# Optimization experiments

Hardware: AMD Instinct MI355X
Metric: run time of the kernel (lower is better)

Reference implementation:

```python
import jax, jax.numpy as jnp
import numpy as np

N_NODES = 10000
LN_EPS = 1e-5


def _gcn(x, W, b, src, dst):
    # GraphConvolution: linear transform then sum-aggregate messages over edges.
    sup = x @ W                               # [B, N, H]
    msg = sup[:, src, :]                      # [B, E, H] gather from source nodes
    agg = jax.vmap(lambda m: jax.ops.segment_sum(m, dst, num_segments=N_NODES))(msg)
    return agg + b


def _layernorm(x, g, b):
    mu = jnp.mean(x, axis=-1, keepdims=True)
    var = jnp.var(x, axis=-1, keepdims=True)
    return (x - mu) * jax.lax.rsqrt(var + LN_EPS) * g + b


def _attention_pool(x, W, u, num_iterations=3):
    # x: [B, N, d] -> r: [B, 1, d]
    a = jnp.tanh(x @ W) @ u                   # [B, N]
    alpha = jax.nn.softmax(a, axis=1)
    r = jnp.einsum('bn,bnd->bd', alpha, x)
    for _ in range(num_iterations):
        beta = jax.nn.softmax(jnp.einsum('bnd,bd->bn', x, r), axis=1)
        r = jnp.einsum('bn,bnd->bd', beta, x)
    return r[:, None, :]


def _forward(x, src, dst, W_conv0, b_conv0, W_convs, b_convs,
             mW1, mb1, mW2, mb2, mW3, mb3,
             ln1_g, ln1_b, ln2_g, ln2_b, attnW, attnu, fW1, fb1, fW2, fb2,
             fcW, fcb):
    gelu = lambda t: jax.nn.gelu(t, approximate=False)
    # stacked GCN layers (first layer distinct input dim)
    x = gelu(_gcn(x, W_conv0, b_conv0, src, dst))
    for i in range(W_convs.shape[0]):
        x = gelu(_gcn(x, W_convs[i], b_convs[i], src, dst))
    # dropout is identity in eval mode
    # MLP head
    x = jax.nn.relu(x @ mW1 + mb1)
    x = jax.nn.relu(x @ mW2 + mb2)
    x = x @ mW3 + mb3
    # Encoder: 2 layers of (attention-pool residual + LN + FFN residual + LN)
    for i in range(2):
        x = x + _attention_pool(x, attnW[i], attnu[i])   # broadcast [B,1,d]
        x = _layernorm(x, ln1_g[i], ln1_b[i])
        h = jax.nn.relu(x @ fW1[i] + fb1[i]) @ fW2[i] + fb2[i]
        x = _layernorm(x + h, ln2_g[i], ln2_b[i])
    x = x @ fcW + fcb                          # [B, N, out]
    return x.mean(axis=1)                      # [B, out]


def setup_inputs() -> dict:
    key = jax.random.key(0)
    ks = jax.random.split(key, 32)
    B, N, E = 4, N_NODES, 160000
    F_in, H, D, A, OUT = 128, 256, 256, 8, 10
    s = lambda k, *shape: jax.random.normal(k, shape, jnp.float32) * 0.05
    return {
        'x': jax.random.normal(ks[0], (B, N, F_in), jnp.float32),
        'src': jax.random.randint(ks[1], (E,), 0, N, jnp.int32),
        'dst': jax.random.randint(ks[2], (E,), 0, N, jnp.int32),
        'W_conv0': s(ks[3], F_in, H), 'b_conv0': s(ks[4], H),
        'W_convs': s(ks[5], 3, H, H), 'b_convs': s(ks[6], 3, H),
        'mW1': s(ks[7], H, H // 2), 'mb1': s(ks[8], H // 2),
        'mW2': s(ks[9], H // 2, H // 4), 'mb2': s(ks[10], H // 4),
        'mW3': s(ks[11], H // 4, D), 'mb3': s(ks[12], D),
        'ln1_g': jnp.ones((2, D), jnp.float32), 'ln1_b': jnp.zeros((2, D), jnp.float32),
        'ln2_g': jnp.ones((2, D), jnp.float32), 'ln2_b': jnp.zeros((2, D), jnp.float32),
        'attnW': s(ks[13], 2, D, A), 'attnu': s(ks[14], 2, A),
        'fW1': s(ks[15], 2, D, H), 'fb1': s(ks[16], 2, H),
        'fW2': s(ks[17], 2, H, D), 'fb2': s(ks[18], 2, D),
        'fcW': s(ks[19], D, OUT), 'fcb': s(ks[20], OUT),
    }


def reference(x, src, dst, W_conv0, b_conv0, W_convs, b_convs,
              mW1, mb1, mW2, mb2, mW3, mb3,
              ln1_g, ln1_b, ln2_g, ln2_b, attnW, attnu, fW1, fb1, fW2, fb2,
              fcW, fcb):
    return _forward(x, src, dst, W_conv0, b_conv0, W_convs, b_convs,
                    mW1, mb1, mW2, mb2, mW3, mb3,
                    ln1_g, ln1_b, ln2_g, ln2_b, attnW, attnu, fW1, fb1, fW2, fb2,
                    fcW, fcb)
```

## Files before the change

kernel.cpp:

```cpp
#include <hip/hip_runtime.h>
#include <math.h>

#define NN 10000
#define NB 4
#define NE 160000
#define DM 256
#define MR (NB * NN)
#define LN_EPS 1e-5f
#define PCH 40
#define NCH (NN / PCH)
#define CCH 100

typedef __attribute__((ext_vector_type(8))) short short8;
typedef __attribute__((ext_vector_type(4))) float floatx4;
typedef __attribute__((ext_vector_type(2))) float f32x2;


__device__ inline float bf2f(unsigned short u) {
    unsigned int x = ((unsigned int)u) << 16;
    float f;
    __builtin_memcpy(&f, &x, 4);
    return f;
}

__device__ inline unsigned short f2bf(float f) {
    unsigned int x;
    __builtin_memcpy(&x, &f, 4);
    unsigned int r = x + 0x7FFFu + ((x >> 16) & 1u);
    return (unsigned short)(r >> 16);
}

__device__ inline float gelu_exact(float x) {
    return 0.5f * x * (1.0f + erff(x * 0.70710678118654752f));
}

__device__ inline float waveAllReduce(float v) {
#pragma unroll
    for (int off = 32; off > 0; off >>= 1) v += __shfl_xor(v, off, 64);
    return v;
}

__device__ inline float group16Reduce(float v) {
#pragma unroll
    for (int off = 8; off > 0; off >>= 1) v += __shfl_xor(v, off, 64);
    return v;
}

__device__ inline void gld16(const unsigned short* g, unsigned short* l) {
    __builtin_amdgcn_global_load_lds((const __attribute__((address_space(1))) void*)g,
                                     (__attribute__((address_space(3))) void*)l, 16, 0, 0);
}


__global__ void zero_i32_kernel(int* p, int n) {
    int i = blockIdx.x * 256 + threadIdx.x;
    if (i < n) p[i] = 0;
}

__global__ void cvt_bf16_kernel(const float* __restrict__ in, unsigned short* __restrict__ out, int n) {
    int i = blockIdx.x * 256 + threadIdx.x;
    if (i < n) out[i] = f2bf(in[i]);
}

struct TD { const float* src; unsigned short* dst; int K; int N; };
struct TDs { TD d[11]; };

__global__ void transpose_all_kernel(TDs tds) {
    TD t = tds.d[blockIdx.y];
    int idx = blockIdx.x * 256 + threadIdx.x;
    int total = t.K * t.N;
    if (idx < total) {
        int n = idx / t.K;
        int k = idx - n * t.K;
        t.dst[idx] = f2bf(t.src[(size_t)k * t.N + n]);
    }
}


__global__ void hist_kernel(const int* __restrict__ dst, int* __restrict__ counts, int e) {
    int i = blockIdx.x * 256 + threadIdx.x;
    if (i < e) atomicAdd(&counts[dst[i]], 1);
}

__global__ __launch_bounds__(256) void scan_kernel(const int* __restrict__ counts,
                                                   int* __restrict__ row_ptr,
                                                   int* __restrict__ fill_pos, int n) {
    __shared__ int sums[256];
    int tid = threadIdx.x;
    int chunk = (n + 255) / 256;
    int s0 = tid * chunk;
    int s1 = min(n, s0 + chunk);
    int local = 0;
    for (int i = s0; i < s1; i++) local += counts[i];
    sums[tid] = local;
    __syncthreads();
    for (int off = 1; off < 256; off <<= 1) {
        int v = (tid >= off) ? sums[tid - off] : 0;
        __syncthreads();
        sums[tid] += v;
        __syncthreads();
    }
    int base = (tid == 0) ? 0 : sums[tid - 1];
    for (int i = s0; i < s1; i++) {
        row_ptr[i] = base;
        fill_pos[i] = base;
        base += counts[i];
    }
    if (tid == 255) row_ptr[n] = sums[255];
}

__global__ void fill_kernel(const int* __restrict__ src, const int* __restrict__ dst,
                            int* __restrict__ fill_pos, int* __restrict__ csr_boff, int e) {
    int i = blockIdx.x * 256 + threadIdx.x;
    if (i < e) {
        int p = atomicAdd(&fill_pos[dst[i]], 1);
        csr_boff[p] = src[i] * (NB * DM * 2);
    }
}


template <int BN, int CM, int K>
__global__ __launch_bounds__(256) void mfma_gemm_kernel(
    const unsigned short* __restrict__ A, const unsigned short* __restrict__ Bt,
    const float* __restrict__ bias, void* __restrict__ Cp, int N, int act) {
    constexpr int NBF = BN / 32;
    constexpr int NI = K / 32;
    __shared__ unsigned short AsL[2][4 * 64 * 8];
    __shared__ unsigned short BsL[2][(BN / 16) * 64 * 8];

    const int tid = threadIdx.x;
    const int w = tid >> 6, l = tid & 63;
    const int wm = w >> 1, wn = w & 1;
    const int bm0 = blockIdx.y * 64;
    const int bn0 = blockIdx.x * BN;
    const int lm = l & 15, lq = l >> 4;

    floatx4 acc[2][NBF];
#pragma unroll
    for (int mi = 0; mi < 2; mi++)
#pragma unroll
        for (int ni = 0; ni < NBF; ni++) acc[mi][ni] = (floatx4){0.f, 0.f, 0.f, 0.f};

    const int a_row = bm0 + (tid >> 6) * 16 + (l & 15);
    const int s_kc = (l >> 4) * 8;
    int b_rown[BN / 64], b_kc[BN / 64];
#pragma unroll
    for (int cc = 0; cc < BN / 64; cc++) {
        int c = tid + cc * 256;
        b_rown[cc] = bn0 + (c >> 6) * 16 + (c & 15);
        b_kc[cc] = ((c & 63) >> 4) * 8;
    }

    gld16(&A[(size_t)a_row * K + s_kc], &AsL[0][tid * 8]);
#pragma unroll
    for (int cc = 0; cc < BN / 64; cc++) {
        int c = tid + cc * 256;
        gld16(&Bt[(size_t)b_rown[cc] * K + b_kc[cc]], &BsL[0][c * 8]);
    }

#pragma unroll
    for (int i = 0; i < NI; i++) {
        const int buf = i & 1;
        __syncthreads();
        if (i + 1 < NI) {
            int k0 = (i + 1) * 32;
            gld16(&A[(size_t)a_row * K + k0 + s_kc], &AsL[buf ^ 1][tid * 8]);
#pragma unroll
            for (int cc = 0; cc < BN / 64; cc++) {
                int c = tid + cc * 256;
                gld16(&Bt[(size_t)b_rown[cc] * K + k0 + b_kc[cc]], &BsL[buf ^ 1][c * 8]);
            }
        }
        short8 af[2], bfv[NBF];
#pragma unroll
        for (int mi = 0; mi < 2; mi++) af[mi] = *(short8*)&AsL[buf][((wm * 2 + mi) * 64 + l) * 8];
#pragma unroll
        for (int ni = 0; ni < NBF; ni++) bfv[ni] = *(short8*)&BsL[buf][((wn * NBF + ni) * 64 + l) * 8];
#pragma unroll
        for (int mi = 0; mi < 2; mi++)
#pragma unroll
            for (int ni = 0; ni < NBF; ni++)
                acc[mi][ni] = __builtin_amdgcn_mfma_f32_16x16x32_bf16(af[mi], bfv[ni], acc[mi][ni], 0, 0, 0);
    }

#pragma unroll
    for (int ni = 0; ni < NBF; ni++) {
        int col = bn0 + (wn * NBF + ni) * 16 + lm;
        float bv = bias ? bias[col] : 0.0f;
#pragma unroll
        for (int mi = 0; mi < 2; mi++) {
            int row0 = bm0 + (wm * 2 + mi) * 16 + lq * 4;
#pragma unroll
            for (int r = 0; r < 4; r++) {
                int row = row0 + r;
                float v = acc[mi][ni][r] + bv;
                if (act == 1) v = fmaxf(v, 0.0f);
                if (CM == 0) {
                    ((float*)Cp)[(size_t)row * N + col] = v;
                } else if (CM == 1) {
                    ((unsigned short*)Cp)[(size_t)row * N + col] = f2bf(v);
                } else {
                    int bb = row / NN;
                    int nn = row - bb * NN;
                    ((unsigned short*)Cp)[(size_t)nn * (NB * DM) + bb * DM + col] = f2bf(v);
                }
            }
        }
    }
}


__global__ __launch_bounds__(256) void gemm_ln_kernel(
    const unsigned short* __restrict__ A,
    const unsigned short* __restrict__ Bt,
    const float* __restrict__ bias,
    const unsigned short* __restrict__ x1,
    const float* __restrict__ g, const float* __restrict__ bt,
    unsigned short* __restrict__ out16) {
    constexpr int K = 256, NBF = 8, NI = K / 32;
    __shared__ unsigned short AsL[2][4 * 64 * 8];
    __shared__ unsigned short BsL[2][16 * 64 * 8];
    __shared__ float rs[2][64], rq[2][64];

    const int tid = threadIdx.x;
    const int w = tid >> 6, l = tid & 63;
    const int wm = w >> 1, wn = w & 1;
    const int bm0 = blockIdx.x * 64;
    const int lm = l & 15, lq = l >> 4;

    floatx4 acc[2][NBF];
#pragma unroll
    for (int mi = 0; mi < 2; mi++)
#pragma unroll
        for (int ni = 0; ni < NBF; ni++) acc[mi][ni] = (floatx4){0.f, 0.f, 0.f, 0.f};

    const int a_row = bm0 + (tid >> 6) * 16 + (l & 15);
    const int s_kc = (l >> 4) * 8;
    int b_rown[4], b_kc[4];
#pragma unroll
    for (int cc = 0; cc < 4; cc++) {
        int c = tid + cc * 256;
        b_rown[cc] = (c >> 6) * 16 + (c & 15);
        b_kc[cc] = ((c & 63) >> 4) * 8;
    }

    gld16(&A[(size_t)a_row * K + s_kc], &AsL[0][tid * 8]);
#pragma unroll
    for (int cc = 0; cc < 4; cc++) {
        int c = tid + cc * 256;
        gld16(&Bt[(size_t)b_rown[cc] * K + b_kc[cc]], &BsL[0][c * 8]);
    }

#pragma unroll
    for (int i = 0; i < NI; i++) {
        const int buf = i & 1;
        __syncthreads();
        if (i + 1 < NI) {
            int k0 = (i + 1) * 32;
            gld16(&A[(size_t)a_row * K + k0 + s_kc], &AsL[buf ^ 1][tid * 8]);
#pragma unroll
            for (int cc = 0; cc < 4; cc++) {
                int c = tid + cc * 256;
                gld16(&Bt[(size_t)b_rown[cc] * K + k0 + b_kc[cc]], &BsL[buf ^ 1][c * 8]);
            }
        }
        short8 af[2], bfv[NBF];
#pragma unroll
        for (int mi = 0; mi < 2; mi++) af[mi] = *(short8*)&AsL[buf][((wm * 2 + mi) * 64 + l) * 8];
#pragma unroll
        for (int ni = 0; ni < NBF; ni++) bfv[ni] = *(short8*)&BsL[buf][((wn * NBF + ni) * 64 + l) * 8];
#pragma unroll
        for (int mi = 0; mi < 2; mi++)
#pragma unroll
            for (int ni = 0; ni < NBF; ni++)
                acc[mi][ni] = __builtin_amdgcn_mfma_f32_16x16x32_bf16(af[mi], bfv[ni], acc[mi][ni], 0, 0, 0);
    }

    float fb[NBF], gv[NBF], bv[NBF];
#pragma unroll
    for (int ni = 0; ni < NBF; ni++) {
        int col = (wn * NBF + ni) * 16 + lm;
        fb[ni] = bias[col];
        gv[ni] = g[col];
        bv[ni] = bt[col];
    }
    float psum[2][4], psq[2][4];
#pragma unroll
    for (int mi = 0; mi < 2; mi++)
#pragma unroll
        for (int r = 0; r < 4; r++) { psum[mi][r] = 0.f; psq[mi][r] = 0.f; }

#pragma unroll
    for (int mi = 0; mi < 2; mi++) {
        int row0 = bm0 + (wm * 2 + mi) * 16 + lq * 4;
#pragma unroll
        for (int r = 0; r < 4; r++) {
#pragma unroll
            for (int ni = 0; ni < NBF; ni++) {
                int col = (wn * NBF + ni) * 16 + lm;
                float y = bf2f(x1[(size_t)(row0 + r) * DM + col]) + acc[mi][ni][r] + fb[ni];
                acc[mi][ni][r] = y;
                psum[mi][r] += y;
                psq[mi][r] += y * y;
            }
        }
    }
#pragma unroll
    for (int mi = 0; mi < 2; mi++)
#pragma unroll
        for (int r = 0; r < 4; r++) {
            float s = group16Reduce(psum[mi][r]);
            float q = group16Reduce(psq[mi][r]);
            if (lm == 0) {
                int rl = (wm * 2 + mi) * 16 + lq * 4 + r;
                rs[wn][rl] = s;
                rq[wn][rl] = q;
            }
        }
    __syncthreads();
#pragma unroll
    for (int mi = 0; mi < 2; mi++) {
        int row0 = bm0 + (wm * 2 + mi) * 16 + lq * 4;
#pragma unroll
        for (int r = 0; r < 4; r++) {
            int rl = (wm * 2 + mi) * 16 + lq * 4 + r;
            float s = rs[0][rl] + rs[1][rl];
            float q = rq[0][rl] + rq[1][rl];
            float mean = s * (1.0f / 256.0f);
            float var = q * (1.0f / 256.0f) - mean * mean;
            float rstd = rsqrtf(var + LN_EPS);
#pragma unroll
            for (int ni = 0; ni < NBF; ni++) {
                int col = (wn * NBF + ni) * 16 + lm;
                out16[(size_t)(row0 + r) * DM + col] =
                    f2bf((acc[mi][ni][r] - mean) * rstd * gv[ni] + bv[ni]);
            }
        }
    }
}


__global__ __launch_bounds__(256) void agg_kernel(const unsigned short* __restrict__ sup,
                                                  const int* __restrict__ row_ptr,
                                                  const int* __restrict__ csr_boff,
                                                  const float* __restrict__ bias,
                                                  unsigned short* __restrict__ out) {
    const char* supc = (const char*)sup;
    int slice = blockIdx.x & 7;
    int grp = blockIdx.x >> 3;
    int w = threadIdx.x >> 6, l = threadIdx.x & 63;
    int n = grp * 4 + w;
    int s = __builtin_amdgcn_readfirstlane(row_ptr[n]);
    int e = __builtin_amdgcn_readfirstlane(row_ptr[n + 1]);
    const int lane_off = slice * 256 + l * 4;
    f32x2 acc = {0.f, 0.f};
    int j = s;
    for (; j + 8 <= e; j += 8) {
        int off[8];
#pragma unroll
        for (int k = 0; k < 8; k++) off[k] = csr_boff[j + k];
        unsigned int v[8];
#pragma unroll
        for (int k = 0; k < 8; k++)
            v[k] = *(const unsigned int*)(supc + (unsigned)(off[k] + lane_off));
#pragma unroll
        for (int k = 0; k < 8; k++) {
            unsigned int lo = v[k] << 16;
            unsigned int hi = v[k] & 0xFFFF0000u;
            float fx, fy;
            __builtin_memcpy(&fx, &lo, 4);
            __builtin_memcpy(&fy, &hi, 4);
            f32x2 t = {fx, fy};
            acc += t;
        }
    }
    for (; j < e; j++) {
        unsigned int v = *(const unsigned int*)(supc + (unsigned)(csr_boff[j] + lane_off));
        unsigned int lo = v << 16;
        unsigned int hi = v & 0xFFFF0000u;
        float fx, fy;
        __builtin_memcpy(&fx, &lo, 4);
        __builtin_memcpy(&fy, &hi, 4);
        f32x2 t = {fx, fy};
        acc += t;
    }
    int gdim = slice * 128 + l * 2;
    int b = gdim >> 8;
    int d = gdim & 255;
    float2 bv = *(const float2*)&bias[d];
    ushort2 o;
    o.x = f2bf(gelu_exact(acc[0] + bv.x));
    o.y = f2bf(gelu_exact(acc[1] + bv.y));
    *(ushort2*)&out[((size_t)b * NN + n) * DM + d] = o;
}


template <int MODE>
__global__ __launch_bounds__(256) void attn_pool_kernel(const unsigned short* __restrict__ x16,
                                                        const float* __restrict__ W,
                                                        const float* __restrict__ u,
                                                        const float* __restrict__ r_in,
                                                        float* __restrict__ pm,
                                                        float* __restrict__ pl,
                                                        float* __restrict__ pv) {
    int c = blockIdx.x, b = blockIdx.y;
    int tid = threadIdx.x, w = tid >> 6, l = tid & 63;
    float4 rv = {0, 0, 0, 0};
    float u0[8];
    if (MODE == 1) {
        rv = *(const float4*)&r_in[b * DM + l * 4];
    } else {
#pragma unroll
        for (int j = 0; j < 8; j++) u0[j] = u[j];
    }
    int n0 = c * PCH;
    float m = -INFINITY, L = 0.0f;
    float v0 = 0.f, v1 = 0.f, v2 = 0.f, v3 = 0.f;
    for (int n = n0 + w; n < n0 + PCH; n += 4) {
        ushort4 xb = *(const ushort4*)&x16[((size_t)b * NN + n) * DM + l * 4];
        float x0 = bf2f(xb.x), x1 = bf2f(xb.y), x2 = bf2f(xb.z), x3 = bf2f(xb.w);
        float s;
        if (MODE == 1) {
            s = x0 * rv.x + x1 * rv.y + x2 * rv.z + x3 * rv.w;
            s = waveAllReduce(s);
        } else {
            const float4* Wv = (const float4*)W;
            int d0 = l * 4;
            float xs[4] = {x0, x1, x2, x3};
            float t[8] = {0, 0, 0, 0, 0, 0, 0, 0};
#pragma unroll
            for (int dd = 0; dd < 4; dd++) {
                float4 w0 = Wv[(d0 + dd) * 2 + 0];
                float4 w1 = Wv[(d0 + dd) * 2 + 1];
                t[0] += xs[dd] * w0.x; t[1] += xs[dd] * w0.y; t[2] += xs[dd] * w0.z; t[3] += xs[dd] * w0.w;
                t[4] += xs[dd] * w1.x; t[5] += xs[dd] * w1.y; t[6] += xs[dd] * w1.z; t[7] += xs[dd] * w1.w;
            }
#pragma unroll
            for (int jj = 0; jj < 8; jj++) t[jj] = waveAllReduce(t[jj]);
            s = 0.f;
#pragma unroll
            for (int jj = 0; jj < 8; jj++) s += tanhf(t[jj]) * u0[jj];
        }
        if (s > m) {
            float sc = __expf(m - s);
            L *= sc; v0 *= sc; v1 *= sc; v2 *= sc; v3 *= sc;
            m = s;
        }
        float wgt = __expf(s - m);
        L += wgt;
        v0 += wgt * x0; v1 += wgt * x1; v2 += wgt * x2; v3 += wgt * x3;
    }
    __shared__ float sm[4], sl[4];
    __shared__ float sv[4][DM];
    if (l == 0) { sm[w] = m; sl[w] = L; }
    float4 vv = {v0, v1, v2, v3};
    *(float4*)&sv[w][l * 4] = vv;
    __syncthreads();
    int d = tid;
    float M = fmaxf(fmaxf(sm[0], sm[1]), fmaxf(sm[2], sm[3]));
    float e0 = __expf(sm[0] - M), e1 = __expf(sm[1] - M);
    float e2 = __expf(sm[2] - M), e3 = __expf(sm[3] - M);
    float Lt = e0 * sl[0] + e1 * sl[1] + e2 * sl[2] + e3 * sl[3];
    float vd = e0 * sv[0][d] + e1 * sv[1][d] + e2 * sv[2][d] + e3 * sv[3][d];
    pv[((size_t)b * NCH + c) * DM + d] = vd;
    if (d == 0) {
        pm[b * NCH + c] = M;
        pl[b * NCH + c] = Lt;
    }
}

__global__ __launch_bounds__(256) void attn_combine_kernel(const float* __restrict__ pm,
                                                           const float* __restrict__ pl,
                                                           const float* __restrict__ pv,
                                                           float* __restrict__ r) {
    int b = blockIdx.x, tid = threadIdx.x;
    __shared__ float red[256];
    __shared__ float se[NCH];
    float mv = -INFINITY;
    for (int c = tid; c < NCH; c += 256) mv = fmaxf(mv, pm[b * NCH + c]);
    red[tid] = mv;
    __syncthreads();
    for (int off = 128; off > 0; off >>= 1) {
        if (tid < off) red[tid] = fmaxf(red[tid], red[tid + off]);
        __syncthreads();
    }
    float M = red[0];
    __syncthreads();
    float lsum = 0.0f;
    for (int c = tid; c < NCH; c += 256) {
        float e = __expf(pm[b * NCH + c] - M);
        se[c] = e;
        lsum += e * pl[b * NCH + c];
    }
    red[tid] = lsum;
    __syncthreads();
    for (int off = 128; off > 0; off >>= 1) {
        if (tid < off) red[tid] += red[tid + off];
        __syncthreads();
    }
    float L = red[0];
    __syncthreads();
    float acc = 0.0f;
    for (int c = 0; c < NCH; c++) acc += se[c] * pv[((size_t)b * NCH + c) * DM + tid];
    r[b * DM + tid] = acc / L;
}


__global__ __launch_bounds__(256) void ln_bcast_kernel(const unsigned short* __restrict__ x16,
                                                       const float* __restrict__ r,
                                                       const float* __restrict__ g,
                                                       const float* __restrict__ bt,
                                                       unsigned short* __restrict__ out16) {
    int l = threadIdx.x & 63, w = threadIdx.x >> 6;
    int row = blockIdx.x * 4 + w;
    int b = row / NN;
    ushort4 xb = *(const ushort4*)&x16[(size_t)row * DM + l * 4];
    float4 rv = *(const float4*)(r + (size_t)b * DM + l * 4);
    float4 y;
    y.x = bf2f(xb.x) + rv.x; y.y = bf2f(xb.y) + rv.y;
    y.z = bf2f(xb.z) + rv.z; y.w = bf2f(xb.w) + rv.w;
    float s = y.x + y.y + y.z + y.w;
    float sq = y.x * y.x + y.y * y.y + y.z * y.z + y.w * y.w;
    s = waveAllReduce(s);
    sq = waveAllReduce(sq);
    float mean = s * (1.0f / 256.0f);
    float var = sq * (1.0f / 256.0f) - mean * mean;
    float rstd = rsqrtf(var + LN_EPS);
    float4 gv = *(const float4*)(g + l * 4);
    float4 bv = *(const float4*)(bt + l * 4);
    ushort4 o;
    o.x = f2bf((y.x - mean) * rstd * gv.x + bv.x);
    o.y = f2bf((y.y - mean) * rstd * gv.y + bv.y);
    o.z = f2bf((y.z - mean) * rstd * gv.z + bv.z);
    o.w = f2bf((y.w - mean) * rstd * gv.w + bv.w);
    *(ushort4*)&out16[(size_t)row * DM + l * 4] = o;
}


__global__ __launch_bounds__(256) void colsum_kernel(const unsigned short* __restrict__ x16,
                                                     float* __restrict__ pcol) {
    int b = blockIdx.y, c = blockIdx.x, d = threadIdx.x;
    int n0 = c * CCH, n1 = n0 + CCH;
    float acc = 0.0f;
    for (int n = n0; n < n1; n++) acc += bf2f(x16[((size_t)b * NN + n) * DM + d]);
    pcol[((size_t)b * (NN / CCH) + c) * DM + d] = acc;
}

__global__ __launch_bounds__(256) void final_kernel(const float* __restrict__ pcol,
                                                    const float* __restrict__ fcW,
                                                    const float* __restrict__ fcb,
                                                    float* __restrict__ out) {
    int b = blockIdx.x, d = threadIdx.x;
    __shared__ float sx[DM];
    float acc = 0.0f;
    for (int c = 0; c < NN / CCH; c++) acc += pcol[((size_t)b * (NN / CCH) + c) * DM + d];
    sx[d] = acc;
    __syncthreads();
    if (d < 10) {
        float o = 0.0f;
        for (int k = 0; k < DM; k++) o += sx[k] * fcW[k * 10 + d];
        out[b * 10 + d] = o * (1.0f / NN) + fcb[d];
    }
}


extern "C" void kernel_launch(void* const* d_in, const int* in_sizes, int n_in,
                              void* d_out, int out_size, void* d_ws, size_t ws_size,
                              hipStream_t stream) {
    const float* x_in    = (const float*)d_in[0];
    const int*   src     = (const int*)d_in[1];
    const int*   dst     = (const int*)d_in[2];
    const float* W_conv0 = (const float*)d_in[3];
    const float* b_conv0 = (const float*)d_in[4];
    const float* W_convs = (const float*)d_in[5];
    const float* b_convs = (const float*)d_in[6];
    const float* mW1 = (const float*)d_in[7];
    const float* mb1 = (const float*)d_in[8];
    const float* mW2 = (const float*)d_in[9];
    const float* mb2 = (const float*)d_in[10];
    const float* mW3 = (const float*)d_in[11];
    const float* mb3 = (const float*)d_in[12];
    const float* ln1_g = (const float*)d_in[13];
    const float* ln1_b = (const float*)d_in[14];
    const float* ln2_g = (const float*)d_in[15];
    const float* ln2_b = (const float*)d_in[16];
    const float* attnW = (const float*)d_in[17];
    const float* attnu = (const float*)d_in[18];
    const float* fW1 = (const float*)d_in[19];
    const float* fb1 = (const float*)d_in[20];
    const float* fW2 = (const float*)d_in[21];
    const float* fb2 = (const float*)d_in[22];
    const float* fcW = (const float*)d_in[23];
    const float* fcb = (const float*)d_in[24];
    float* out = (float*)d_out;

    char* p = (char*)d_ws;
    auto alloc = [&](size_t bytes) { char* q = p; p += (bytes + 255) & ~(size_t)255; return q; };
    unsigned short* sup16 = (unsigned short*)alloc((size_t)MR * DM * 2);
    unsigned short* act16 = (unsigned short*)alloc((size_t)MR * DM * 2);
    unsigned short* b16   = (unsigned short*)alloc((size_t)MR * DM * 2);
    unsigned short* t1    = (unsigned short*)alloc((size_t)MR * 128 * 2);
    unsigned short* t2    = (unsigned short*)alloc((size_t)MR * 64 * 2);
    unsigned short* wt    = (unsigned short*)alloc((size_t)548864 * 2);
    float* rbuf = (float*)alloc(NB * DM * 4);
    float* pm0  = (float*)alloc(NB * NCH * 4);
    float* pl0  = (float*)alloc(NB * NCH * 4);
    float* pv0  = (float*)alloc((size_t)NB * NCH * DM * 4);
    float* pcol = (float*)alloc((size_t)NB * (NN / CCH) * DM * 4);
    int* counts   = (int*)alloc(NN * 4);
    int* row_ptr  = (int*)alloc((NN + 1) * 4);
    int* fill_pos = (int*)alloc(NN * 4);
    int* csr_boff = (int*)alloc(NE * 4);

    unsigned short* Wt_conv0 = wt;
    unsigned short* Wt_convs = Wt_conv0 + 32768;
    unsigned short* mW1t = Wt_convs + 196608;
    unsigned short* mW2t = mW1t + 32768;
    unsigned short* mW3t = mW2t + 8192;
    unsigned short* fW1t = mW3t + 16384;
    unsigned short* fW2t = fW1t + 131072;

    const dim3 blk(256);

    zero_i32_kernel<<<(NN + 255) / 256, blk, 0, stream>>>(counts, NN);
    hist_kernel<<<(NE + 255) / 256, blk, 0, stream>>>(dst, counts, NE);
    scan_kernel<<<1, blk, 0, stream>>>(counts, row_ptr, fill_pos, NN);
    fill_kernel<<<(NE + 255) / 256, blk, 0, stream>>>(src, dst, fill_pos, csr_boff, NE);

    TDs tds;
    tds.d[0]  = {W_conv0, Wt_conv0, 128, 256};
    tds.d[1]  = {W_convs + 0 * 65536, Wt_convs + 0 * 65536, 256, 256};
    tds.d[2]  = {W_convs + 1 * 65536, Wt_convs + 1 * 65536, 256, 256};
    tds.d[3]  = {W_convs + 2 * 65536, Wt_convs + 2 * 65536, 256, 256};
    tds.d[4]  = {mW1, mW1t, 256, 128};
    tds.d[5]  = {mW2, mW2t, 128, 64};
    tds.d[6]  = {mW3, mW3t, 64, 256};
    tds.d[7]  = {fW1 + 0 * 65536, fW1t + 0 * 65536, 256, 256};
    tds.d[8]  = {fW1 + 1 * 65536, fW1t + 1 * 65536, 256, 256};
    tds.d[9]  = {fW2 + 0 * 65536, fW2t + 0 * 65536, 256, 256};
    tds.d[10] = {fW2 + 1 * 65536, fW2t + 1 * 65536, 256, 256};
    transpose_all_kernel<<<dim3(256, 11), blk, 0, stream>>>(tds);

    cvt_bf16_kernel<<<(MR * 128 + 255) / 256, blk, 0, stream>>>(x_in, t1, MR * 128);

    mfma_gemm_kernel<256, 2, 128><<<dim3(1, MR / 64), blk, 0, stream>>>(t1, Wt_conv0, nullptr, sup16, 256, 0);
    agg_kernel<<<NN * 2, blk, 0, stream>>>(sup16, row_ptr, csr_boff, b_conv0, act16);
    for (int i = 0; i < 3; i++) {
        mfma_gemm_kernel<256, 2, 256><<<dim3(1, MR / 64), blk, 0, stream>>>(act16, Wt_convs + (size_t)i * 65536, nullptr, sup16, 256, 0);
        agg_kernel<<<NN * 2, blk, 0, stream>>>(sup16, row_ptr, csr_boff, b_convs + (size_t)i * 256, act16);
    }

    mfma_gemm_kernel<128, 1, 256><<<dim3(1, MR / 64), blk, 0, stream>>>(act16, mW1t, mb1, t1, 128, 1);
    mfma_gemm_kernel<64, 1, 128><<<dim3(1, MR / 64), blk, 0, stream>>>(t1, mW2t, mb2, t2, 64, 1);
    mfma_gemm_kernel<256, 1, 64><<<dim3(1, MR / 64), blk, 0, stream>>>(t2, mW3t, mb3, act16, 256, 0);

    const dim3 poolGrid(NCH, NB);
    for (int i = 0; i < 2; i++) {
        const float* Wp = attnW + (size_t)i * DM * 8;
        const float* up = attnu + (size_t)i * 8;
        attn_pool_kernel<0><<<poolGrid, blk, 0, stream>>>(act16, Wp, up, nullptr, pm0, pl0, pv0);
        attn_combine_kernel<<<NB, blk, 0, stream>>>(pm0, pl0, pv0, rbuf);
        for (int it = 0; it < 3; it++) {
            attn_pool_kernel<1><<<poolGrid, blk, 0, stream>>>(act16, nullptr, nullptr, rbuf, pm0, pl0, pv0);
            attn_combine_kernel<<<NB, blk, 0, stream>>>(pm0, pl0, pv0, rbuf);
        }
        ln_bcast_kernel<<<MR / 4, blk, 0, stream>>>(act16, rbuf, ln1_g + (size_t)i * DM,
                                                    ln1_b + (size_t)i * DM, b16);
        mfma_gemm_kernel<256, 1, 256><<<dim3(1, MR / 64), blk, 0, stream>>>(b16, fW1t + (size_t)i * 65536,
                                                                            fb1 + (size_t)i * DM, sup16, 256, 1);
        gemm_ln_kernel<<<MR / 64, blk, 0, stream>>>(sup16, fW2t + (size_t)i * 65536,
                                                    fb2 + (size_t)i * DM, b16,
                                                    ln2_g + (size_t)i * DM, ln2_b + (size_t)i * DM,
                                                    act16);
    }

    colsum_kernel<<<dim3(NN / CCH, NB), blk, 0, stream>>>(act16, pcol);
    final_kernel<<<NB, blk, 0, stream>>>(pcol, fcW, fcb, out);
}
```

Before: 733.0 us.

## Retile large GEMMs to 128x128 with 512-thread blocks and fuse prologue kernels

The GEMM template gains a BM parameter, and the 256-wide GCN and FFN1 GEMMs now run as 128x128 tiles with 512-thread blocks on a 2D grid instead of 64x256 tiles. Buffers are padded by 64 rows and stores are guarded for the ragged last M tile. Separately, the zero, weight-transpose and input-convert kernels are merged into one prologue launch to cut launch overhead. The new tiling changes the reuse balance between A and B loads and the occupancy per CU, and it adds bounds checks plus reads of padded rows.

```diff
diff --git a/kernel.cpp b/kernel.cpp
--- a/kernel.cpp
+++ b/kernel.cpp
@@ -6,6 +6,7 @@
 #define NE 160000
 #define DM 256
 #define MR (NB * NN)
+#define MRP (MR + 64)
 #define LN_EPS 1e-5f
 #define PCH 40
 #define NCH (NN / PCH)
@@ -52,28 +53,34 @@
 }
 
 
-__global__ void zero_i32_kernel(int* p, int n) {
-    int i = blockIdx.x * 256 + threadIdx.x;
-    if (i < n) p[i] = 0;
-}
-
-__global__ void cvt_bf16_kernel(const float* __restrict__ in, unsigned short* __restrict__ out, int n) {
-    int i = blockIdx.x * 256 + threadIdx.x;
-    if (i < n) out[i] = f2bf(in[i]);
-}
-
 struct TD { const float* src; unsigned short* dst; int K; int N; };
 struct TDs { TD d[11]; };
 
-__global__ void transpose_all_kernel(TDs tds) {
-    TD t = tds.d[blockIdx.y];
-    int idx = blockIdx.x * 256 + threadIdx.x;
-    int total = t.K * t.N;
-    if (idx < total) {
-        int n = idx / t.K;
-        int k = idx - n * t.K;
-        t.dst[idx] = f2bf(t.src[(size_t)k * t.N + n]);
-    }
+__global__ __launch_bounds__(256) void prologue_kernel(TDs tds,
+                                                       const float* __restrict__ x_in,
+                                                       unsigned short* __restrict__ xout,
+                                                       int* __restrict__ counts) {
+    int bid = blockIdx.x, tid = threadIdx.x;
+    if (bid < 40) {
+        int i = bid * 256 + tid;
+        if (i < NN) counts[i] = 0;
+        return;
+    }
+    bid -= 40;
+    if (bid < 2816) {
+        TD t = tds.d[bid >> 8];
+        int idx = (bid & 255) * 256 + tid;
+        int total = t.K * t.N;
+        if (idx < total) {
+            int n = idx / t.K;
+            int k = idx - n * t.K;
+            t.dst[idx] = f2bf(t.src[(size_t)k * t.N + n]);
+        }
+        return;
+    }
+    bid -= 2816;
+    int i = bid * 256 + tid;
+    xout[i] = f2bf(x_in[i]);
 }
 
 
@@ -119,19 +126,20 @@
 }
 
 
-template <int BN, int CM, int K>
-__global__ __launch_bounds__(256) void mfma_gemm_kernel(
+template <int BM, int BN, int CM, int K>
+__global__ __launch_bounds__(BM * 4) void mfma_gemm_kernel(
     const unsigned short* __restrict__ A, const unsigned short* __restrict__ Bt,
     const float* __restrict__ bias, void* __restrict__ Cp, int N, int act) {
     constexpr int NBF = BN / 32;
     constexpr int NI = K / 32;
-    __shared__ unsigned short AsL[2][4 * 64 * 8];
+    constexpr int NT = BM * 4;
+    __shared__ unsigned short AsL[2][(BM / 16) * 64 * 8];
     __shared__ unsigned short BsL[2][(BN / 16) * 64 * 8];
 
     const int tid = threadIdx.x;
     const int w = tid >> 6, l = tid & 63;
     const int wm = w >> 1, wn = w & 1;
-    const int bm0 = blockIdx.y * 64;
+    const int bm0 = blockIdx.y * BM;
     const int bn0 = blockIdx.x * BN;
     const int lm = l & 15, lq = l >> 4;
 
@@ -143,18 +151,19 @@
 
     const int a_row = bm0 + (tid >> 6) * 16 + (l & 15);
     const int s_kc = (l >> 4) * 8;
-    int b_rown[BN / 64], b_kc[BN / 64];
-#pragma unroll
-    for (int cc = 0; cc < BN / 64; cc++) {
-        int c = tid + cc * 256;
+    constexpr int BCC = (BN * 4 + NT - 1) / NT;
+    int b_rown[BCC], b_kc[BCC];
+#pragma unroll
+    for (int cc = 0; cc < BCC; cc++) {
+        int c = tid + cc * NT;
         b_rown[cc] = bn0 + (c >> 6) * 16 + (c & 15);
         b_kc[cc] = ((c & 63) >> 4) * 8;
     }
 
     gld16(&A[(size_t)a_row * K + s_kc], &AsL[0][tid * 8]);
 #pragma unroll
-    for (int cc = 0; cc < BN / 64; cc++) {
-        int c = tid + cc * 256;
+    for (int cc = 0; cc < BCC; cc++) {
+        int c = tid + cc * NT;
         gld16(&Bt[(size_t)b_rown[cc] * K + b_kc[cc]], &BsL[0][c * 8]);
     }
 
@@ -166,8 +175,8 @@
             int k0 = (i + 1) * 32;
             gld16(&A[(size_t)a_row * K + k0 + s_kc], &AsL[buf ^ 1][tid * 8]);
 #pragma unroll
-            for (int cc = 0; cc < BN / 64; cc++) {
-                int c = tid + cc * 256;
+            for (int cc = 0; cc < BCC; cc++) {
+                int c = tid + cc * NT;
                 gld16(&Bt[(size_t)b_rown[cc] * K + k0 + b_kc[cc]], &BsL[buf ^ 1][c * 8]);
             }
         }
@@ -193,16 +202,18 @@
 #pragma unroll
             for (int r = 0; r < 4; r++) {
                 int row = row0 + r;
-                float v = acc[mi][ni][r] + bv;
-                if (act == 1) v = fmaxf(v, 0.0f);
-                if (CM == 0) {
-                    ((float*)Cp)[(size_t)row * N + col] = v;
-                } else if (CM == 1) {
-                    ((unsigned short*)Cp)[(size_t)row * N + col] = f2bf(v);
-                } else {
-                    int bb = row / NN;
-                    int nn = row - bb * NN;
-                    ((unsigned short*)Cp)[(size_t)nn * (NB * DM) + bb * DM + col] = f2bf(v);
+                if (row < MR) {
+                    float v = acc[mi][ni][r] + bv;
+                    if (act == 1) v = fmaxf(v, 0.0f);
+                    if (CM == 0) {
+                        ((float*)Cp)[(size_t)row * N + col] = v;
+                    } else if (CM == 1) {
+                        ((unsigned short*)Cp)[(size_t)row * N + col] = f2bf(v);
+                    } else {
+                        int bb = row / NN;
+                        int nn = row - bb * NN;
+                        ((unsigned short*)Cp)[(size_t)nn * (NB * DM) + bb * DM + col] = f2bf(v);
+                    }
                 }
             }
         }
@@ -596,11 +607,11 @@
 
     char* p = (char*)d_ws;
     auto alloc = [&](size_t bytes) { char* q = p; p += (bytes + 255) & ~(size_t)255; return q; };
-    unsigned short* sup16 = (unsigned short*)alloc((size_t)MR * DM * 2);
-    unsigned short* act16 = (unsigned short*)alloc((size_t)MR * DM * 2);
-    unsigned short* b16   = (unsigned short*)alloc((size_t)MR * DM * 2);
-    unsigned short* t1    = (unsigned short*)alloc((size_t)MR * 128 * 2);
-    unsigned short* t2    = (unsigned short*)alloc((size_t)MR * 64 * 2);
+    unsigned short* sup16 = (unsigned short*)alloc((size_t)MRP * DM * 2);
+    unsigned short* act16 = (unsigned short*)alloc((size_t)MRP * DM * 2);
+    unsigned short* b16   = (unsigned short*)alloc((size_t)MRP * DM * 2);
+    unsigned short* t1    = (unsigned short*)alloc((size_t)MRP * 128 * 2);
+    unsigned short* t2    = (unsigned short*)alloc((size_t)MRP * 64 * 2);
     unsigned short* wt    = (unsigned short*)alloc((size_t)548864 * 2);
     float* rbuf = (float*)alloc(NB * DM * 4);
     float* pm0  = (float*)alloc(NB * NCH * 4);
@@ -621,11 +632,6 @@
     unsigned short* fW2t = fW1t + 131072;
 
     const dim3 blk(256);
-
-    zero_i32_kernel<<<(NN + 255) / 256, blk, 0, stream>>>(counts, NN);
-    hist_kernel<<<(NE + 255) / 256, blk, 0, stream>>>(dst, counts, NE);
-    scan_kernel<<<1, blk, 0, stream>>>(counts, row_ptr, fill_pos, NN);
-    fill_kernel<<<(NE + 255) / 256, blk, 0, stream>>>(src, dst, fill_pos, csr_boff, NE);
 
     TDs tds;
     tds.d[0]  = {W_conv0, Wt_conv0, 128, 256};
@@ -639,20 +645,25 @@
     tds.d[8]  = {fW1 + 1 * 65536, fW1t + 1 * 65536, 256, 256};
     tds.d[9]  = {fW2 + 0 * 65536, fW2t + 0 * 65536, 256, 256};
     tds.d[10] = {fW2 + 1 * 65536, fW2t + 1 * 65536, 256, 256};
-    transpose_all_kernel<<<dim3(256, 11), blk, 0, stream>>>(tds);
-
-    cvt_bf16_kernel<<<(MR * 128 + 255) / 256, blk, 0, stream>>>(x_in, t1, MR * 128);
-
-    mfma_gemm_kernel<256, 2, 128><<<dim3(1, MR / 64), blk, 0, stream>>>(t1, Wt_conv0, nullptr, sup16, 256, 0);
+    prologue_kernel<<<40 + 2816 + (MR * 128) / 256, blk, 0, stream>>>(tds, x_in, t1, counts);
+
+    hist_kernel<<<(NE + 255) / 256, blk, 0, stream>>>(dst, counts, NE);
+    scan_kernel<<<1, blk, 0, stream>>>(counts, row_ptr, fill_pos, NN);
+    fill_kernel<<<(NE + 255) / 256, blk, 0, stream>>>(src, dst, fill_pos, csr_boff, NE);
+
+    const dim3 big128(2, (MR + 127) / 128);
+    const dim3 blk512(512);
+
+    mfma_gemm_kernel<128, 128, 2, 128><<<big128, blk512, 0, stream>>>(t1, Wt_conv0, nullptr, sup16, 256, 0);
     agg_kernel<<<NN * 2, blk, 0, stream>>>(sup16, row_ptr, csr_boff, b_conv0, act16);
     for (int i = 0; i < 3; i++) {
-        mfma_gemm_kernel<256, 2, 256><<<dim3(1, MR / 64), blk, 0, stream>>>(act16, Wt_convs + (size_t)i * 65536, nullptr, sup16, 256, 0);
+        mfma_gemm_kernel<128, 128, 2, 256><<<big128, blk512, 0, stream>>>(act16, Wt_convs + (size_t)i * 65536, nullptr, sup16, 256, 0);
         agg_kernel<<<NN * 2, blk, 0, stream>>>(sup16, row_ptr, csr_boff, b_convs + (size_t)i * 256, act16);
     }
 
-    mfma_gemm_kernel<128, 1, 256><<<dim3(1, MR / 64), blk, 0, stream>>>(act16, mW1t, mb1, t1, 128, 1);
-    mfma_gemm_kernel<64, 1, 128><<<dim3(1, MR / 64), blk, 0, stream>>>(t1, mW2t, mb2, t2, 64, 1);
-    mfma_gemm_kernel<256, 1, 64><<<dim3(1, MR / 64), blk, 0, stream>>>(t2, mW3t, mb3, act16, 256, 0);
+    mfma_gemm_kernel<64, 128, 1, 256><<<dim3(1, MR / 64), blk, 0, stream>>>(act16, mW1t, mb1, t1, 128, 1);
+    mfma_gemm_kernel<64, 64, 1, 128><<<dim3(1, MR / 64), blk, 0, stream>>>(t1, mW2t, mb2, t2, 64, 1);
+    mfma_gemm_kernel<64, 256, 1, 64><<<dim3(1, MR / 64), blk, 0, stream>>>(t2, mW3t, mb3, act16, 256, 0);
 
     const dim3 poolGrid(NCH, NB);
     for (int i = 0; i < 2; i++) {
@@ -666,8 +677,8 @@
         }
         ln_bcast_kernel<<<MR / 4, blk, 0, stream>>>(act16, rbuf, ln1_g + (size_t)i * DM,
                                                     ln1_b + (size_t)i * DM, b16);
-        mfma_gemm_kernel<256, 1, 256><<<dim3(1, MR / 64), blk, 0, stream>>>(b16, fW1t + (size_t)i * 65536,
-                                                                            fb1 + (size_t)i * DM, sup16, 256, 1);
+        mfma_gemm_kernel<128, 128, 1, 256><<<big128, blk512, 0, stream>>>(b16, fW1t + (size_t)i * 65536,
+                                                                          fb1 + (size_t)i * DM, sup16, 256, 1);
         gemm_ln_kernel<<<MR / 64, blk, 0, stream>>>(sup16, fW2t + (size_t)i * 65536,
                                                     fb2 + (size_t)i * DM, b16,
                                                     ln2_g + (size_t)i * DM, ln2_b + (size_t)i * DM,
```

Result: no change. 744.1 us (+1.5%).
